# Kernel tuning notes

Measured on AMD Instinct MI355X. Metric: run time of the kernel, lower is better.

Reference implementation:

```python
import jax, jax.numpy as jnp
import numpy as np

BS, IMG, P, GRID, NPATCH = 4, 224, 14, 16, 256
D, HID, NC, NDIST = 384, 2688, 1000, 7
BETA = 0.07
LN_EPS = 1e-6


def setup_inputs() -> dict:
    key = jax.random.key(0)
    ks = jax.random.split(key, 10)
    feat_target = jax.random.normal(ks[0], (BS, NPATCH, D), jnp.float32)
    feat_ref = jax.random.normal(ks[1], (BS, NPATCH, D), jnp.float32)
    labels_ref = jax.random.randint(ks[2], (BS, 1, IMG, IMG), 0, NC, jnp.int32)
    # distractor permutations of the batch (one per distractor sample)
    perms = jnp.argsort(jax.random.uniform(ks[3], (NDIST, BS)), axis=-1).astype(jnp.int32)
    # projector Mlp (fc1 -> GELU -> fc2), xavier-ish scaling
    fc1_w = jax.random.normal(ks[4], (D, HID), jnp.float32) * (1.0 / np.sqrt(D))
    fc1_b = jnp.zeros((HID,), jnp.float32)
    fc2_w = jax.random.normal(ks[5], (HID, D), jnp.float32) * (1.0 / np.sqrt(HID))
    fc2_b = jnp.zeros((D,), jnp.float32)
    ln_w = jnp.ones((D,), jnp.float32)
    ln_b = jnp.zeros((D,), jnp.float32)
    return {"feat_target": feat_target, "feat_ref": feat_ref, "labels_ref": labels_ref,
            "perms": perms, "fc1_w": fc1_w, "fc1_b": fc1_b, "fc2_w": fc2_w,
            "fc2_b": fc2_b, "ln_w": ln_w, "ln_b": ln_b}


def _layer_norm(x, w, b):
    mu = x.mean(-1, keepdims=True)
    var = jnp.mean((x - mu) ** 2, axis=-1, keepdims=True)
    return (x - mu) * jax.lax.rsqrt(var + LN_EPS) * w + b


def _l2norm(x, eps=1e-12):
    n = jnp.sqrt(jnp.sum(x * x, axis=-1, keepdims=True))
    return x / jnp.maximum(n, eps)


def reference(feat_target, feat_ref, labels_ref, perms, fc1_w, fc1_b, fc2_w, fc2_b, ln_w, ln_b):
    bs = feat_target.shape[0]

    def proj_norm(x):
        h = jax.nn.gelu(x @ fc1_w + fc1_b, approximate=False)  # torch nn.GELU (erf)
        return _layer_norm(h @ fc2_w + fc2_b, ln_w, ln_b)

    ft = proj_norm(feat_target)   # (bs, 256, 384)
    fr = proj_norm(feat_ref)      # (bs, 256, 384)

    # patchify ground truth: (bs,1,224,224) -> (bs, 256, 14*14)
    g = labels_ref.reshape(bs, 1, GRID, P, GRID, P).transpose(0, 2, 4, 1, 3, 5)
    g = g.reshape(bs, NPATCH, P * P)
    # per-patch class histogram / (P*P) == one_hot(...).mean(dim=3), without huge one-hot
    seg = (jnp.arange(NPATCH, dtype=jnp.int32)[None, :, None] * NC + g).reshape(bs, -1)
    counts = jax.vmap(lambda s: jax.ops.segment_sum(
        jnp.ones(s.shape, jnp.float32), s, num_segments=NPATCH * NC))(seg)
    label = counts.reshape(bs, NPATCH, NC) / float(P * P)  # (bs, 256, 1000)

    # distractors: block 0 is identity, blocks 1..NDIST are batch permutations
    all_perm = jnp.concatenate([jnp.arange(bs, dtype=perms.dtype)[None], perms], 0)  # (8, bs)
    lab_d = label[all_perm].transpose(1, 0, 2, 3).reshape(bs, -1, NC)   # (bs, 2048, 1000)
    feat_d = fr[all_perm].transpose(1, 0, 2, 3).reshape(bs, -1, D)      # (bs, 2048, 384)

    # cosine-similarity softmax cross attention (soft kNN over labels)
    q = _l2norm(ft)
    k = _l2norm(feat_d)
    attn = jax.nn.softmax(jnp.einsum('bqd,bkd->bqk', q, k) / BETA, axis=-1)
    label_hat = jnp.einsum('bqk,bkc->bqc', attn, lab_d)                 # (bs, 256, 1000)

    label_hat = label_hat.reshape(bs, GRID, GRID, NC).transpose(0, 3, 1, 2)
    # nearest upsample 16x16 -> 224x224 (scale 14 exactly)
    out = jnp.repeat(jnp.repeat(label_hat, P, axis=2), P, axis=3)
    return out
```

## Files before the change

### kernel.cpp

```cpp
#include <hip/hip_runtime.h>

#define BSZ 4
#define NPATCH 256
#define DIM 384
#define HID 2688
#define NCLS 1000
#define KTOT 2048
#define IMGSZ 224
#define PCH 14
#define GRD 16

static constexpr float INV_BETA = 1.0f / 0.07f;
static constexpr float LN_EPS_F = 1e-6f;

typedef unsigned short u16;
typedef unsigned int   u32;
typedef __attribute__((ext_vector_type(8))) __bf16 bf16x8;
typedef __attribute__((ext_vector_type(4))) float  f32x4;

#define WAITVM(n) asm volatile("s_waitcnt vmcnt(" #n ")" ::: "memory")

__device__ __forceinline__ u16 f2bf(float f) {
    u32 u = __float_as_uint(f);
    return (u16)((u + 0x7FFFu + ((u >> 16) & 1u)) >> 16);
}
__device__ __forceinline__ float bf2f(u16 h) {
    return __uint_as_float(((u32)h) << 16);
}
__device__ __forceinline__ f32x4 mfma16(bf16x8 a, bf16x8 b, f32x4 c) {
    return __builtin_amdgcn_mfma_f32_16x16x32_bf16(a, b, c, 0, 0, 0);
}
__device__ __forceinline__ void gll16(const u16* g, u16* l) {
    __builtin_amdgcn_global_load_lds(
        (const __attribute__((address_space(1))) void*)g,
        (__attribute__((address_space(3))) void*)l, 16, 0, 0);
}
__device__ __forceinline__ bf16x8 ld8(const u16* p) {
    return *(const bf16x8*)p;
}
__device__ __forceinline__ int swz(int row, int cseg) {
    return cseg ^ ((row >> 1) & 3);
}

__device__ __forceinline__ void transpose_cast_body(
    const float* __restrict__ In, int R, int C, int bx, int by,
    u16* __restrict__ OutT, float (*tile)[33])
{
    int cx = bx * 32, ry = by * 32;
    int t = threadIdx.x;
    int tr = t >> 5, tc = t & 31;
    #pragma unroll
    for (int i = 0; i < 4; ++i)
        tile[tr + i * 8][tc] = In[(size_t)(ry + tr + i * 8) * C + cx + tc];
    __syncthreads();
    int a = t >> 3, seg = t & 7;
    u16 h4[4];
    #pragma unroll
    for (int i = 0; i < 4; ++i)
        h4[i] = f2bf(tile[seg * 4 + i][a]);
    size_t off = (size_t)(cx + a) * R + ry + seg * 4;
    *(uint2*)(OutT + off) = make_uint2((u32)h4[0] | ((u32)h4[1] << 16),
                                       (u32)h4[2] | ((u32)h4[3] << 16));
}

__global__ __launch_bounds__(256) void prep_kernel(
    const float* __restrict__ Xt, const float* __restrict__ Xr,
    const float* __restrict__ fc1w, const float* __restrict__ fc2w,
    const int* __restrict__ labels,
    u16* __restrict__ Xbf, u16* __restrict__ W1T, u16* __restrict__ W2T,
    u16* __restrict__ LabT)
{
    __shared__ float tile[32][33];
    __shared__ int hist16[16][NCLS];
    int blk = blockIdx.x, t = threadIdx.x;
    if (blk < 768) {
        int e = (blk * 256 + t) * 4;
        const float* src = (e < 1024 * DIM) ? (Xt + e) : (Xr + e - 1024 * DIM);
        float4 v = *(const float4*)src;
        u16 h[4] = {f2bf(v.x), f2bf(v.y), f2bf(v.z), f2bf(v.w)};
        *(uint2*)(Xbf + e) = make_uint2((u32)h[0] | ((u32)h[1] << 16),
                                        (u32)h[2] | ((u32)h[3] << 16));
    } else if (blk < 1776) {
        int i = blk - 768;
        transpose_cast_body(fc1w, DIM, HID, i % (HID / 32), i / (HID / 32), W1T, tile);
    } else if (blk < 2784) {
        int i = blk - 1776;
        transpose_cast_body(fc2w, HID, DIM, i % (DIM / 32), i / (DIM / 32), W2T, tile);
    } else {
        int bp = blk - 2784;
        int b = bp >> 4, py = bp & 15;
        for (int u = t; u < 16 * NCLS; u += 256) ((int*)hist16)[u] = 0;
        __syncthreads();
        const int* lrow = labels + (size_t)b * IMGSZ * IMGSZ + py * PCH * IMGSZ;
        for (int i = t; i < PCH * IMGSZ; i += 256) {
            int lab = lrow[i];
            int px = (i % IMGSZ) / PCH;
            atomicAdd(&hist16[px][lab], 1);
        }
        __syncthreads();
        const float inv = 1.0f / (PCH * PCH);
        for (int u = t; u < 16 * NCLS; u += 256) {
            int c = u >> 4, px = u & 15;
            LabT[((size_t)(b << 10) + c) * 256 + py * 16 + px] =
                f2bf(hist16[px][c] * inv);
        }
    }
}

template<int MODE>
__global__ __launch_bounds__(256) void gemm64(
    const u16* __restrict__ A_g, const u16* __restrict__ B_g,
    const float* __restrict__ bias,
    u16* __restrict__ OutB, float* __restrict__ OutF)
{
    constexpr int K  = (MODE == 1) ? HID : DIM;
    constexpr int KS = (MODE == 1) ? HID / 4 : K;
    constexpr int NT = KS / 32;
    constexpr int N  = (MODE == 0) ? HID : DIM;

    __shared__ u16 As[3][128 * 32];
    __shared__ u16 Bs[3][64 * 32];

    const int tid = threadIdx.x, lane = tid & 63, wid = tid >> 6;
    const int wm = wid >> 1, wn = wid & 1;
    int n0, m0;
    if constexpr (MODE == 0) {
        int s = (blockIdx.x & 7) * 84 + (blockIdx.x >> 3);
        n0 = (s % 42) * 64;
        m0 = (s / 42) * 128;
    } else {
        n0 = blockIdx.x * 64;
        m0 = blockIdx.y * 128;
    }

    const int kbase = (MODE == 1) ? blockIdx.z * KS : 0;
    const u16* a_g = A_g + (size_t)m0 * K + kbase;
    const u16* b_g = B_g + (size_t)n0 * K + kbase;

    auto stage = [&](int buf, int k0) {
        #pragma unroll
        for (int j = 0; j < 2; ++j) {
            int g = j * 256 + tid;
            int row = g >> 2, cs = g & 3;
            int col = swz(row, cs) << 3;
            gll16(a_g + (size_t)row * K + k0 + col, &As[buf][g * 8]);
        }
        {
            int row = tid >> 2, cs = tid & 3;
            int col = swz(row, cs) << 3;
            gll16(b_g + (size_t)row * K + k0 + col, &Bs[buf][tid * 8]);
        }
    };

    const int l15 = lane & 15, cq = lane >> 4;
    int aoff[4], boff[2];
    #pragma unroll
    for (int i = 0; i < 4; ++i) {
        int ra = wm * 64 + i * 16 + l15;
        aoff[i] = ra * 32 + swz(ra, cq) * 8;
    }
    #pragma unroll
    for (int j = 0; j < 2; ++j) {
        int rb = wn * 32 + j * 16 + l15;
        boff[j] = rb * 32 + swz(rb, cq) * 8;
    }

    f32x4 acc[4][2] = {};

    auto compute = [&](int buf) {
        bf16x8 a[4], bb[2];
        #pragma unroll
        for (int i = 0; i < 4; ++i) a[i] = ld8(&As[buf][aoff[i]]);
        #pragma unroll
        for (int j = 0; j < 2; ++j) bb[j] = ld8(&Bs[buf][boff[j]]);
        #pragma unroll
        for (int mi = 0; mi < 4; ++mi)
            #pragma unroll
            for (int ni = 0; ni < 2; ++ni)
                acc[mi][ni] = mfma16(a[mi], bb[ni], acc[mi][ni]);
    };

    stage(0, 0);
    stage(1, 32);
    int cur = 0;
    for (int t = 0; t < NT - 1; ++t) {
        WAITVM(3);
        __builtin_amdgcn_s_barrier();
        __builtin_amdgcn_sched_barrier(0);
        if (t + 2 < NT) {
            int nb = cur + 2; if (nb >= 3) nb -= 3;
            stage(nb, (t + 2) * 32);
        }
        compute(cur);
        cur = (cur == 2) ? 0 : cur + 1;
    }
    WAITVM(0);
    __builtin_amdgcn_s_barrier();
    __builtin_amdgcn_sched_barrier(0);
    compute(cur);

    #pragma unroll
    for (int mi = 0; mi < 4; ++mi)
        #pragma unroll
        for (int ni = 0; ni < 2; ++ni)
            #pragma unroll
            for (int r = 0; r < 4; ++r) {
                int gm = m0 + wm * 64 + mi * 16 + cq * 4 + r;
                int gn = n0 + wn * 32 + ni * 16 + l15;
                float v = acc[mi][ni][r];
                if constexpr (MODE == 0) {
                    v += bias[gn];
                    v = 0.5f * v * (1.0f + erff(v * 0.7071067811865476f));
                    OutB[(size_t)gm * N + gn] = f2bf(v);
                } else {
                    OutF[(size_t)blockIdx.z * (2048 * DIM) + (size_t)gm * N + gn] = v;
                }
            }
}

__global__ __launch_bounds__(256) void qk64(
    const u16* __restrict__ Z, const int* __restrict__ perms,
    u16* __restrict__ E, float* __restrict__ R)
{
    constexpr int NT = DIM / 32;
    __shared__ u16 As[3][64 * 32];
    __shared__ u16 Bs[3][64 * 32];

    const int tid = threadIdx.x, lane = tid & 63, wid = tid >> 6;
    const int wm = wid >> 1, wn = wid & 1;
    const int n0 = blockIdx.x * 64, m0 = blockIdx.y * 64, b = blockIdx.z;
    const int d = n0 >> 8;
    const int apd = (d == 0) ? b : perms[(d - 1) * BSZ + b];

    const u16* a_g = Z + (size_t)(b * NPATCH + m0) * DIM;
    const u16* b_g = Z + (size_t)(1024 + apd * NPATCH + (n0 & 255)) * DIM;

    auto stage = [&](int buf, int k0) {
        int row = tid >> 2, cs = tid & 3;
        int col = swz(row, cs) << 3;
        gll16(a_g + (size_t)row * DIM + k0 + col, &As[buf][tid * 8]);
        gll16(b_g + (size_t)row * DIM + k0 + col, &Bs[buf][tid * 8]);
    };

    const int l15 = lane & 15, cq = lane >> 4;
    int aoff[2], boff[2];
    #pragma unroll
    for (int i = 0; i < 2; ++i) {
        int ra = wm * 32 + i * 16 + l15;
        aoff[i] = ra * 32 + swz(ra, cq) * 8;
        int rb = wn * 32 + i * 16 + l15;
        boff[i] = rb * 32 + swz(rb, cq) * 8;
    }

    f32x4 acc[2][2] = {};
    auto compute = [&](int buf) {
        bf16x8 a[2], bb[2];
        #pragma unroll
        for (int i = 0; i < 2; ++i) {
            a[i] = ld8(&As[buf][aoff[i]]);
            bb[i] = ld8(&Bs[buf][boff[i]]);
        }
        #pragma unroll
        for (int mi = 0; mi < 2; ++mi)
            #pragma unroll
            for (int ni = 0; ni < 2; ++ni)
                acc[mi][ni] = mfma16(a[mi], bb[ni], acc[mi][ni]);
    };

    stage(0, 0);
    stage(1, 32);
    int cur = 0;
    for (int t = 0; t < NT - 1; ++t) {
        WAITVM(2);
        __builtin_amdgcn_s_barrier();
        __builtin_amdgcn_sched_barrier(0);
        if (t + 2 < NT) {
            int nb = cur + 2; if (nb >= 3) nb -= 3;
            stage(nb, (t + 2) * 32);
        }
        compute(cur);
        cur = (cur == 2) ? 0 : cur + 1;
    }
    WAITVM(0);
    __builtin_amdgcn_s_barrier();
    __builtin_amdgcn_sched_barrier(0);
    compute(cur);

    float rp[2][4] = {};
    #pragma unroll
    for (int mi = 0; mi < 2; ++mi)
        #pragma unroll
        for (int ni = 0; ni < 2; ++ni)
            #pragma unroll
            for (int r = 0; r < 4; ++r) {
                int gm = m0 + wm * 32 + mi * 16 + cq * 4 + r;
                int gn = n0 + wn * 32 + ni * 16 + l15;
                float e = expf((acc[mi][ni][r] - 1.0f) * INV_BETA);
                u16 h = f2bf(e);
                E[((size_t)b * NPATCH + gm) * KTOT + gn] = h;
                rp[mi][r] += bf2f(h);
            }
    #pragma unroll
    for (int mi = 0; mi < 2; ++mi)
        #pragma unroll
        for (int r = 0; r < 4; ++r) {
            float v = rp[mi][r];
            #pragma unroll
            for (int off = 1; off < 16; off <<= 1) v += __shfl_xor(v, off);
            if (l15 == 0) {
                int gm = m0 + wm * 32 + mi * 16 + cq * 4 + r;
                atomicAdd(&R[(size_t)b * NPATCH + gm], v);
            }
        }
}

__global__ __launch_bounds__(256) void pv64(
    const u16* __restrict__ E, const u16* __restrict__ LabT,
    const int* __restrict__ perms, float* __restrict__ Lp)
{
    constexpr int KSP = KTOT / 4;
    constexpr int NT  = KSP / 32;
    __shared__ u16 As[3][128 * 32];
    __shared__ u16 Bs[3][64 * 32];

    const int tid = threadIdx.x, lane = tid & 63, wid = tid >> 6;
    const int wm = wid >> 1, wn = wid & 1;
    const int n0 = blockIdx.x * 64, m0 = blockIdx.y * 128;
    const int b = blockIdx.z & 3, ks = blockIdx.z >> 2;
    const int s0 = ks * 2;
    const int apd0 = (s0 == 0) ? b : perms[(s0 - 1) * BSZ + b];
    const int apd1 = perms[s0 * BSZ + b];

    const u16* abase = E + (size_t)(b * NPATCH + m0) * KTOT + ks * KSP;

    auto stage = [&](int buf, int k0) {
        #pragma unroll
        for (int j = 0; j < 2; ++j) {
            int g = j * 256 + tid;
            int row = g >> 2, cs = g & 3;
            int col = swz(row, cs) << 3;
            gll16(abase + (size_t)row * KTOT + k0 + col, &As[buf][g * 8]);
        }
        {
            int apd = (k0 & 256) ? apd1 : apd0;
            int p0 = k0 & 255;
            int row = tid >> 2, cs = tid & 3;
            int col = swz(row, cs) << 3;
            gll16(LabT + ((size_t)(apd << 10) + n0 + row) * 256 + p0 + col,
                  &Bs[buf][tid * 8]);
        }
    };

    const int l15 = lane & 15, cq = lane >> 4;
    int aoff[4], boff[2];
    #pragma unroll
    for (int i = 0; i < 4; ++i) {
        int ra = wm * 64 + i * 16 + l15;
        aoff[i] = ra * 32 + swz(ra, cq) * 8;
    }
    #pragma unroll
    for (int j = 0; j < 2; ++j) {
        int rb = wn * 32 + j * 16 + l15;
        boff[j] = rb * 32 + swz(rb, cq) * 8;
    }

    f32x4 acc[4][2] = {};
    auto compute = [&](int buf) {
        bf16x8 a[4], bb[2];
        #pragma unroll
        for (int i = 0; i < 4; ++i) a[i] = ld8(&As[buf][aoff[i]]);
        #pragma unroll
        for (int j = 0; j < 2; ++j) bb[j] = ld8(&Bs[buf][boff[j]]);
        #pragma unroll
        for (int mi = 0; mi < 4; ++mi)
            #pragma unroll
            for (int ni = 0; ni < 2; ++ni)
                acc[mi][ni] = mfma16(a[mi], bb[ni], acc[mi][ni]);
    };

    stage(0, 0);
    stage(1, 32);
    int cur = 0;
    for (int t = 0; t < NT - 1; ++t) {
        WAITVM(3);
        __builtin_amdgcn_s_barrier();
        __builtin_amdgcn_sched_barrier(0);
        if (t + 2 < NT) {
            int nb = cur + 2; if (nb >= 3) nb -= 3;
            stage(nb, (t + 2) * 32);
        }
        compute(cur);
        cur = (cur == 2) ? 0 : cur + 1;
    }
    WAITVM(0);
    __builtin_amdgcn_s_barrier();
    __builtin_amdgcn_sched_barrier(0);
    compute(cur);

    #pragma unroll
    for (int mi = 0; mi < 4; ++mi)
        #pragma unroll
        for (int ni = 0; ni < 2; ++ni) {
            int gn = n0 + wn * 32 + ni * 16 + l15;
            if (gn < NCLS) {
                #pragma unroll
                for (int r = 0; r < 4; ++r) {
                    int gm = m0 + wm * 64 + mi * 16 + cq * 4 + r;
                    Lp[(((size_t)ks * BSZ + b) * NPATCH + gm) * NCLS + gn] =
                        acc[mi][ni][r];
                }
            }
        }
}

__device__ __forceinline__ float wave_sum(float v) {
    #pragma unroll
    for (int off = 32; off > 0; off >>= 1) v += __shfl_xor(v, off);
    return v;
}

__global__ __launch_bounds__(256) void ln_l2_kernel(
    const float* __restrict__ P0, const float* __restrict__ fc2b,
    const float* __restrict__ w, const float* __restrict__ b,
    u16* __restrict__ Zbf, float* __restrict__ R)
{
    if (blockIdx.x < 256 && threadIdx.x < 4)
        R[blockIdx.x * 4 + threadIdx.x] = 0.0f;
    const float* P1 = P0 + 1 * 2048 * DIM;
    const float* P2 = P0 + 2 * 2048 * DIM;
    const float* P3 = P0 + 3 * 2048 * DIM;
    int wid = threadIdx.x >> 6, lane = threadIdx.x & 63;
    int row = blockIdx.x * 4 + wid;
    size_t base = (size_t)row * DIM;
    float x[6];
    float s = 0.0f;
    #pragma unroll
    for (int i = 0; i < 6; ++i) {
        int c = lane + 64 * i;
        x[i] = ((P0[base + c] + P1[base + c]) + (P2[base + c] + P3[base + c])) + fc2b[c];
        s += x[i];
    }
    s = wave_sum(s);
    float mu = s * (1.0f / DIM);
    float vs = 0.0f;
    #pragma unroll
    for (int i = 0; i < 6; ++i) { float d = x[i] - mu; vs += d * d; }
    vs = wave_sum(vs);
    float rstd = 1.0f / sqrtf(vs * (1.0f / DIM) + LN_EPS_F);
    float z[6];
    float n2 = 0.0f;
    #pragma unroll
    for (int i = 0; i < 6; ++i) {
        z[i] = (x[i] - mu) * rstd * w[lane + 64 * i] + b[lane + 64 * i];
        n2 += z[i] * z[i];
    }
    n2 = wave_sum(n2);
    float inv = 1.0f / fmaxf(sqrtf(n2), 1e-12f);
    #pragma unroll
    for (int i = 0; i < 6; ++i)
        Zbf[base + lane + 64 * i] = f2bf(z[i] * inv);
}

__global__ __launch_bounds__(256) void upsample_kernel(
    const float* __restrict__ Lp, const float* __restrict__ R,
    float* __restrict__ out)
{
    constexpr size_t S = (size_t)BSZ * NPATCH * NCLS;
    int blk = blockIdx.x;
    int gy = blk & 15;
    int bc = blk >> 4;
    int c = bc % NCLS;
    int b = bc / NCLS;
    __shared__ float vals[GRD];
    int t = threadIdx.x;
    if (t < GRD) {
        int q = b * NPATCH + gy * GRD + t;
        size_t i = (size_t)q * NCLS + c;
        vals[t] = ((Lp[i] + Lp[i + S]) + (Lp[i + 2 * S] + Lp[i + 3 * S])) / R[q];
    }
    __syncthreads();
    float* obase = out + ((size_t)(b * NCLS + c) * IMGSZ + gy * PCH) * IMGSZ;
    for (int idx = t; idx < PCH * 56; idx += 256) {
        int x4 = idx % 56, dy = idx / 56;
        int x0 = x4 * 4;
        f32x4 v = {vals[x0 / PCH], vals[(x0 + 1) / PCH],
                   vals[(x0 + 2) / PCH], vals[(x0 + 3) / PCH]};
        __builtin_nontemporal_store(v, (f32x4*)(obase + dy * IMGSZ + x0));
    }
}

extern "C" void kernel_launch(void* const* d_in, const int* in_sizes, int n_in,
                              void* d_out, int out_size, void* d_ws, size_t ws_size,
                              hipStream_t stream)
{
    (void)in_sizes; (void)n_in; (void)out_size; (void)ws_size;
    const float* feat_t = (const float*)d_in[0];
    const float* feat_r = (const float*)d_in[1];
    const int*   labels = (const int*)d_in[2];
    const int*   perms  = (const int*)d_in[3];
    const float* fc1_w  = (const float*)d_in[4];
    const float* fc1_b  = (const float*)d_in[5];
    const float* fc2_w  = (const float*)d_in[6];
    const float* fc2_b  = (const float*)d_in[7];
    const float* ln_w   = (const float*)d_in[8];
    const float* ln_b   = (const float*)d_in[9];
    float* out = (float*)d_out;
    char*  W   = (char*)d_ws;

    u16*   H    = (u16*)(W + 0);
    u16*   E    = (u16*)(W + 0);
    float* R    = (float*)(W + 4194304);
    float* Lp   = (float*)(W + 4718592);
    float* P0   = (float*)(W + 22020096);
    u16*   Zbf  = (u16*)(W + 34603008);
    u16*   LabT = (u16*)(W + 37748736);
    u16*   Xbf  = (u16*)(W + 39845888);
    u16*   W1T  = (u16*)(W + 42991616);
    u16*   W2T  = (u16*)(W + 47120384);

    prep_kernel<<<dim3(2848), dim3(256), 0, stream>>>(
        feat_t, feat_r, fc1_w, fc2_w, labels, Xbf, W1T, W2T, LabT);

    gemm64<0><<<dim3(672), dim3(256), 0, stream>>>(
        Xbf, W1T, fc1_b, H, nullptr);

    gemm64<1><<<dim3(6, 16, 4), dim3(256), 0, stream>>>(
        H, W2T, nullptr, nullptr, P0);

    ln_l2_kernel<<<dim3(2048 / 4), dim3(256), 0, stream>>>(
        P0, fc2_b, ln_w, ln_b, Zbf, R);

    qk64<<<dim3(32, 4, 4), dim3(256), 0, stream>>>(Zbf, perms, E, R);

    pv64<<<dim3(16, 2, 16), dim3(256), 0, stream>>>(E, LabT, perms, Lp);

    upsample_kernel<<<dim3(BSZ * NCLS * GRD), dim3(256), 0, stream>>>(Lp, R, out);
}
```

Baseline: 226.1 us.

## Halve split-K in fc2 and PV, shrink PV tile, split histogram kernel

Split-K factor for the fc2 GEMM drops from 4 to 2 and for the PV GEMM from 4 to 2, so the LayerNorm and upsample kernels read two partial buffers instead of four. The PV kernel now uses 64x64 tiles with a 4-entry shared permutation table, which changes the grid to 16x4x8. The label histogram moves out of prep_kernel into its own kernel. Fewer partial sums mean less partial-buffer traffic and reduction work, at the cost of longer K loops per block and a different balance of occupancy and parallelism.

```diff
diff --git a/kernel.cpp b/kernel.cpp
--- a/kernel.cpp
+++ b/kernel.cpp
@@ -66,12 +66,9 @@
 __global__ __launch_bounds__(256) void prep_kernel(
     const float* __restrict__ Xt, const float* __restrict__ Xr,
     const float* __restrict__ fc1w, const float* __restrict__ fc2w,
-    const int* __restrict__ labels,
-    u16* __restrict__ Xbf, u16* __restrict__ W1T, u16* __restrict__ W2T,
-    u16* __restrict__ LabT)
+    u16* __restrict__ Xbf, u16* __restrict__ W1T, u16* __restrict__ W2T)
 {
     __shared__ float tile[32][33];
-    __shared__ int hist16[16][NCLS];
     int blk = blockIdx.x, t = threadIdx.x;
     if (blk < 768) {
         int e = (blk * 256 + t) * 4;
@@ -83,27 +80,32 @@
     } else if (blk < 1776) {
         int i = blk - 768;
         transpose_cast_body(fc1w, DIM, HID, i % (HID / 32), i / (HID / 32), W1T, tile);
-    } else if (blk < 2784) {
+    } else {
         int i = blk - 1776;
         transpose_cast_body(fc2w, HID, DIM, i % (DIM / 32), i / (DIM / 32), W2T, tile);
-    } else {
-        int bp = blk - 2784;
-        int b = bp >> 4, py = bp & 15;
-        for (int u = t; u < 16 * NCLS; u += 256) ((int*)hist16)[u] = 0;
-        __syncthreads();
-        const int* lrow = labels + (size_t)b * IMGSZ * IMGSZ + py * PCH * IMGSZ;
-        for (int i = t; i < PCH * IMGSZ; i += 256) {
-            int lab = lrow[i];
-            int px = (i % IMGSZ) / PCH;
-            atomicAdd(&hist16[px][lab], 1);
-        }
-        __syncthreads();
-        const float inv = 1.0f / (PCH * PCH);
-        for (int u = t; u < 16 * NCLS; u += 256) {
-            int c = u >> 4, px = u & 15;
-            LabT[((size_t)(b << 10) + c) * 256 + py * 16 + px] =
-                f2bf(hist16[px][c] * inv);
-        }
+    }
+}
+
+__global__ __launch_bounds__(256) void hist_kernel(
+    const int* __restrict__ labels, u16* __restrict__ LabT)
+{
+    __shared__ int hist16[16][NCLS];
+    int bp = blockIdx.x, t = threadIdx.x;
+    int b = bp >> 4, py = bp & 15;
+    for (int u = t; u < 16 * NCLS; u += 256) ((int*)hist16)[u] = 0;
+    __syncthreads();
+    const int* lrow = labels + (size_t)b * IMGSZ * IMGSZ + py * PCH * IMGSZ;
+    for (int i = t; i < PCH * IMGSZ; i += 256) {
+        int lab = lrow[i];
+        int px = (i % IMGSZ) / PCH;
+        atomicAdd(&hist16[px][lab], 1);
+    }
+    __syncthreads();
+    const float inv = 1.0f / (PCH * PCH);
+    for (int u = t; u < 16 * NCLS; u += 256) {
+        int c = u >> 4, px = u & 15;
+        LabT[((size_t)(b << 10) + c) * 256 + py * 16 + px] =
+            f2bf(hist16[px][c] * inv);
     }
 }
 
@@ -114,7 +116,7 @@
     u16* __restrict__ OutB, float* __restrict__ OutF)
 {
     constexpr int K  = (MODE == 1) ? HID : DIM;
-    constexpr int KS = (MODE == 1) ? HID / 4 : K;
+    constexpr int KS = (MODE == 1) ? HID / 2 : K;
     constexpr int NT = KS / 32;
     constexpr int N  = (MODE == 0) ? HID : DIM;
 
@@ -318,61 +320,54 @@
     const u16* __restrict__ E, const u16* __restrict__ LabT,
     const int* __restrict__ perms, float* __restrict__ Lp)
 {
-    constexpr int KSP = KTOT / 4;
+    constexpr int KSP = KTOT / 2;
     constexpr int NT  = KSP / 32;
-    __shared__ u16 As[3][128 * 32];
+    __shared__ u16 As[3][64 * 32];
     __shared__ u16 Bs[3][64 * 32];
+    __shared__ int ap[4];
 
     const int tid = threadIdx.x, lane = tid & 63, wid = tid >> 6;
     const int wm = wid >> 1, wn = wid & 1;
-    const int n0 = blockIdx.x * 64, m0 = blockIdx.y * 128;
+    const int n0 = blockIdx.x * 64, m0 = blockIdx.y * 64;
     const int b = blockIdx.z & 3, ks = blockIdx.z >> 2;
-    const int s0 = ks * 2;
-    const int apd0 = (s0 == 0) ? b : perms[(s0 - 1) * BSZ + b];
-    const int apd1 = perms[s0 * BSZ + b];
+    if (tid < 4) {
+        int s = ks * 4 + tid;
+        ap[tid] = (s == 0) ? b : perms[(s - 1) * BSZ + b];
+    }
+    __syncthreads();
 
     const u16* abase = E + (size_t)(b * NPATCH + m0) * KTOT + ks * KSP;
 
     auto stage = [&](int buf, int k0) {
-        #pragma unroll
-        for (int j = 0; j < 2; ++j) {
-            int g = j * 256 + tid;
-            int row = g >> 2, cs = g & 3;
-            int col = swz(row, cs) << 3;
-            gll16(abase + (size_t)row * KTOT + k0 + col, &As[buf][g * 8]);
-        }
-        {
-            int apd = (k0 & 256) ? apd1 : apd0;
-            int p0 = k0 & 255;
-            int row = tid >> 2, cs = tid & 3;
-            int col = swz(row, cs) << 3;
-            gll16(LabT + ((size_t)(apd << 10) + n0 + row) * 256 + p0 + col,
-                  &Bs[buf][tid * 8]);
-        }
+        int row = tid >> 2, cs = tid & 3;
+        int col = swz(row, cs) << 3;
+        gll16(abase + (size_t)row * KTOT + k0 + col, &As[buf][tid * 8]);
+        int apd = ap[(k0 >> 8) & 3];
+        int p0 = k0 & 255;
+        gll16(LabT + ((size_t)(apd << 10) + n0 + row) * 256 + p0 + col,
+              &Bs[buf][tid * 8]);
     };
 
     const int l15 = lane & 15, cq = lane >> 4;
-    int aoff[4], boff[2];
-    #pragma unroll
-    for (int i = 0; i < 4; ++i) {
-        int ra = wm * 64 + i * 16 + l15;
+    int aoff[2], boff[2];
+    #pragma unroll
+    for (int i = 0; i < 2; ++i) {
+        int ra = wm * 32 + i * 16 + l15;
         aoff[i] = ra * 32 + swz(ra, cq) * 8;
-    }
-    #pragma unroll
-    for (int j = 0; j < 2; ++j) {
-        int rb = wn * 32 + j * 16 + l15;
-        boff[j] = rb * 32 + swz(rb, cq) * 8;
-    }
-
-    f32x4 acc[4][2] = {};
+        int rb = wn * 32 + i * 16 + l15;
+        boff[i] = rb * 32 + swz(rb, cq) * 8;
+    }
+
+    f32x4 acc[2][2] = {};
     auto compute = [&](int buf) {
-        bf16x8 a[4], bb[2];
-        #pragma unroll
-        for (int i = 0; i < 4; ++i) a[i] = ld8(&As[buf][aoff[i]]);
-        #pragma unroll
-        for (int j = 0; j < 2; ++j) bb[j] = ld8(&Bs[buf][boff[j]]);
-        #pragma unroll
-        for (int mi = 0; mi < 4; ++mi)
+        bf16x8 a[2], bb[2];
+        #pragma unroll
+        for (int i = 0; i < 2; ++i) {
+            a[i] = ld8(&As[buf][aoff[i]]);
+            bb[i] = ld8(&Bs[buf][boff[i]]);
+        }
+        #pragma unroll
+        for (int mi = 0; mi < 2; ++mi)
             #pragma unroll
             for (int ni = 0; ni < 2; ++ni)
                 acc[mi][ni] = mfma16(a[mi], bb[ni], acc[mi][ni]);
@@ -382,7 +377,7 @@
     stage(1, 32);
     int cur = 0;
     for (int t = 0; t < NT - 1; ++t) {
-        WAITVM(3);
+        WAITVM(2);
         __builtin_amdgcn_s_barrier();
         __builtin_amdgcn_sched_barrier(0);
         if (t + 2 < NT) {
@@ -398,14 +393,14 @@
     compute(cur);
 
     #pragma unroll
-    for (int mi = 0; mi < 4; ++mi)
+    for (int mi = 0; mi < 2; ++mi)
         #pragma unroll
         for (int ni = 0; ni < 2; ++ni) {
             int gn = n0 + wn * 32 + ni * 16 + l15;
             if (gn < NCLS) {
                 #pragma unroll
                 for (int r = 0; r < 4; ++r) {
-                    int gm = m0 + wm * 64 + mi * 16 + cq * 4 + r;
+                    int gm = m0 + wm * 32 + mi * 16 + cq * 4 + r;
                     Lp[(((size_t)ks * BSZ + b) * NPATCH + gm) * NCLS + gn] =
                         acc[mi][ni][r];
                 }
@@ -426,9 +421,7 @@
 {
     if (blockIdx.x < 256 && threadIdx.x < 4)
         R[blockIdx.x * 4 + threadIdx.x] = 0.0f;
-    const float* P1 = P0 + 1 * 2048 * DIM;
-    const float* P2 = P0 + 2 * 2048 * DIM;
-    const float* P3 = P0 + 3 * 2048 * DIM;
+    const float* P1 = P0 + 2048 * DIM;
     int wid = threadIdx.x >> 6, lane = threadIdx.x & 63;
     int row = blockIdx.x * 4 + wid;
     size_t base = (size_t)row * DIM;
@@ -437,7 +430,7 @@
     #pragma unroll
     for (int i = 0; i < 6; ++i) {
         int c = lane + 64 * i;
-        x[i] = ((P0[base + c] + P1[base + c]) + (P2[base + c] + P3[base + c])) + fc2b[c];
+        x[i] = (P0[base + c] + P1[base + c]) + fc2b[c];
         s += x[i];
     }
     s = wave_sum(s);
@@ -476,7 +469,7 @@
     if (t < GRD) {
         int q = b * NPATCH + gy * GRD + t;
         size_t i = (size_t)q * NCLS + c;
-        vals[t] = ((Lp[i] + Lp[i + S]) + (Lp[i + 2 * S] + Lp[i + 3 * S])) / R[q];
+        vals[t] = (Lp[i] + Lp[i + S]) / R[q];
     }
     __syncthreads();
     float* obase = out + ((size_t)(b * NCLS + c) * IMGSZ + gy * PCH) * IMGSZ;
@@ -518,13 +511,15 @@
     u16*   W1T  = (u16*)(W + 42991616);
     u16*   W2T  = (u16*)(W + 47120384);
 
-    prep_kernel<<<dim3(2848), dim3(256), 0, stream>>>(
-        feat_t, feat_r, fc1_w, fc2_w, labels, Xbf, W1T, W2T, LabT);
+    hist_kernel<<<dim3(64), dim3(256), 0, stream>>>(labels, LabT);
+
+    prep_kernel<<<dim3(2784), dim3(256), 0, stream>>>(
+        feat_t, feat_r, fc1_w, fc2_w, Xbf, W1T, W2T);
 
     gemm64<0><<<dim3(672), dim3(256), 0, stream>>>(
         Xbf, W1T, fc1_b, H, nullptr);
 
-    gemm64<1><<<dim3(6, 16, 4), dim3(256), 0, stream>>>(
+    gemm64<1><<<dim3(6, 16, 2), dim3(256), 0, stream>>>(
         H, W2T, nullptr, nullptr, P0);
 
     ln_l2_kernel<<<dim3(2048 / 4), dim3(256), 0, stream>>>(
@@ -532,7 +527,7 @@
 
     qk64<<<dim3(32, 4, 4), dim3(256), 0, stream>>>(Zbf, perms, E, R);
 
-    pv64<<<dim3(16, 2, 16), dim3(256), 0, stream>>>(E, LabT, perms, Lp);
+    pv64<<<dim3(16, 4, 8), dim3(256), 0, stream>>>(E, LabT, perms, Lp);
 
     upsample_kernel<<<dim3(BSZ * NCLS * GRD), dim3(256), 0, stream>>>(Lp, R, out);
 }
```

After: 232.8 us. 3.0% more time.
